# Optimization experiments

Hardware: AMD Instinct MI355X
Metric: run time of the kernel (lower is better)

The kernel has to match this reference:

```python
import jax, jax.numpy as jnp
import numpy as np

IN_CHANNELS = 512
NUM_HEADS = 8
HEAD_CH = IN_CHANNELS // NUM_HEADS


def setup_inputs() -> dict:
    key = jax.random.key(0)
    k0, k1, k2, k3, k4 = jax.random.split(key, 5)
    B, C, H, W = 4, IN_CHANNELS, 128, 128
    x = jax.random.normal(k0, (B, C, H, W), dtype=jnp.float32)
    # 1x1 Conv2d weights == per-pixel linear layers over channels
    s_in = 1.0 / np.sqrt(C)
    Wqkv = jax.random.uniform(k1, (3 * C, C), dtype=jnp.float32, minval=-s_in, maxval=s_in)
    bqkv = jax.random.uniform(k2, (3 * C,), dtype=jnp.float32, minval=-s_in, maxval=s_in)
    Wout = jax.random.uniform(k3, (C, C), dtype=jnp.float32, minval=-s_in, maxval=s_in)
    bout = jax.random.uniform(k4, (C,), dtype=jnp.float32, minval=-s_in, maxval=s_in)
    return {"x": x, "Wqkv": Wqkv, "bqkv": bqkv, "Wout": Wout, "bout": bout}


def _axial_attention(x, Wqkv, bqkv, Wout, bout):
    B, C, H, W = x.shape
    nh, d = NUM_HEADS, HEAD_CH
    scale = 1.0 / jnp.sqrt(jnp.asarray(d, dtype=x.dtype))

    # 1x1 conv qkv projection: [B, 3C, H, W]
    qkv = jnp.einsum('bchw,oc->bohw', x, Wqkv) + bqkv[None, :, None, None]
    q, k, v = jnp.split(qkv, 3, axis=1)
    # [B, nh, d, H, W]
    q = q.reshape(B, nh, d, H, W)
    k = k.reshape(B, nh, d, H, W)
    v = v.reshape(B, nh, d, H, W)

    # Row attention: for each row h, attend across width (w over u)
    scores_row = jnp.einsum('bndhw,bndhu->bnhwu', q, k) * scale  # [B,nh,H,W,W]
    probs_row = jax.nn.softmax(scores_row, axis=-1)
    out_row = jnp.einsum('bnhwu,bndhu->bndhw', probs_row, v)  # [B,nh,d,H,W]

    # Column attention: for each column w, attend across height (h over g)
    scores_col = jnp.einsum('bndhw,bndgw->bnwhg', q, k) * scale  # [B,nh,W,H,H]
    probs_col = jax.nn.softmax(scores_col, axis=-1)
    out_col = jnp.einsum('bnwhg,bndgw->bndhw', probs_col, v)  # [B,nh,d,H,W]

    out = (out_row + out_col).reshape(B, C, H, W)
    # 1x1 conv output projection
    return jnp.einsum('bchw,oc->bohw', out, Wout) + bout[None, :, None, None]


def reference(x, Wqkv, bqkv, Wout, bout):
    return _axial_attention(x, Wqkv, bqkv, Wout, bout)
```

## Files before the change

kernel.cpp:

```cpp
#include <hip/hip_runtime.h>

#define DI __device__ __forceinline__

typedef __attribute__((ext_vector_type(4))) float f32x4;
typedef __attribute__((ext_vector_type(8))) short s16x8;
typedef __attribute__((ext_vector_type(4))) short s16x4;
typedef unsigned short u16;

#define AS_G(p) ((const __attribute__((address_space(1))) void*)(p))
#define AS_L(p) ((__attribute__((address_space(3))) void*)(p))

DI short f2bf(float f) {
  union { float f; unsigned u; } v; v.f = f;
  unsigned r = v.u + 0x7FFFu + ((v.u >> 16) & 1u);
  return (short)(r >> 16);
}
DI float bf2f(short h) {
  union { unsigned u; float f; } v; v.u = ((unsigned)(u16)h) << 16; return v.f;
}

#define MFMA(a, b, c) __builtin_amdgcn_mfma_f32_16x16x32_bf16((a), (b), (c), 0, 0, 0)

__global__ void cast_weights_kernel(const float* __restrict__ wqkv, u16* __restrict__ wqkv_bf,
                                    const float* __restrict__ wout, u16* __restrict__ wout_bf) {
  const int n1 = 1536 * 512 / 4, n2 = 512 * 512 / 4;
  for (int c = blockIdx.x * blockDim.x + threadIdx.x; c < n1 + n2; c += gridDim.x * blockDim.x) {
    const float4* src; u16* dst; int idx;
    if (c < n1) { src = (const float4*)wqkv; dst = wqkv_bf; idx = c; }
    else        { src = (const float4*)wout; dst = wout_bf; idx = c - n1; }
    float4 v = src[idx];
    s16x4 o;
    o[0] = f2bf(v.x); o[1] = f2bf(v.y); o[2] = f2bf(v.z); o[3] = f2bf(v.w);
    *(s16x4*)(dst + (long)idx * 4) = o;
  }
}

template<bool IN_F32>
__global__ __launch_bounds__(256)
void transpose_kernel(const void* __restrict__ in, u16* __restrict__ out,
                      int in_rstride, int out_rstride, long plane_in, long plane_out) {
  __shared__ __align__(16) u16 t[64][72];
  const int tid = threadIdx.x;
  const long bi = (long)blockIdx.z * plane_in;
  const long bo = (long)blockIdx.z * plane_out;
  const int r0 = blockIdx.y * 64, c0 = blockIdx.x * 64;
#pragma unroll
  for (int i = 0; i < 4; ++i) {
    int c = tid + i * 256;
    int row = c >> 4, c4 = c & 15;
    s16x4 pk;
    if (IN_F32) {
      const float4 v = *(const float4*)((const float*)in + bi + (long)(r0 + row) * in_rstride + c0 + c4 * 4);
      pk[0] = f2bf(v.x); pk[1] = f2bf(v.y); pk[2] = f2bf(v.z); pk[3] = f2bf(v.w);
    } else {
      pk = *(const s16x4*)((const u16*)in + bi + (long)(r0 + row) * in_rstride + c0 + c4 * 4);
    }
    *(s16x4*)&t[row][c4 * 4] = pk;
  }
  __syncthreads();
#pragma unroll
  for (int i = 0; i < 2; ++i) {
    int c = tid + i * 256;
    int orow = c >> 3, u = c & 7;
    s16x8 pk;
#pragma unroll
    for (int j = 0; j < 8; ++j) pk[j] = (short)t[u * 8 + j][orow];
    *(s16x8*)(out + bo + (long)(c0 + orow) * out_rstride + r0 + u * 8) = pk;
  }
}

template<int EPI>
__global__ __launch_bounds__(512, 2)
void gemm_kernel(const u16* __restrict__ A, const u16* __restrict__ B,
                 const float* __restrict__ bias,
                 u16* __restrict__ out_qk, u16* __restrict__ out_v,
                 float* __restrict__ out_f) {
  __shared__ __align__(16) u16 smem[65536];
  const int tid = threadIdx.x;
  const int lane = tid & 63, wid = tid >> 6;
  const int l15 = lane & 15, g4 = lane >> 4;
  const int wr = wid >> 2, wc = wid & 3;
  const int m0 = blockIdx.y * 256, n0 = blockIdx.x * 256;
  const int z = blockIdx.z;
  const u16* Bp = B + (long)z * 8388608;

  f32x4 acc[8][4];
#pragma unroll
  for (int i = 0; i < 8; ++i)
#pragma unroll
    for (int j = 0; j < 4; ++j) { f32x4 z4 = {0.f, 0.f, 0.f, 0.f}; acc[i][j] = z4; }

  auto stage = [&](int kt, int buf) {
    u16* As = smem + buf * 32768;
    u16* Bs = As + 16384;
#pragma unroll
    for (int i = 0; i < 4; ++i) {
      int unit = tid + i * 512;
      int row = unit >> 3;
      int csw = ((unit & 7) ^ (row & 7)) * 8;
      __builtin_amdgcn_global_load_lds(AS_G(A + (long)(m0 + row) * 512 + kt * 64 + csw),
                                       AS_L(As + unit * 8), 16, 0, 0);
    }
#pragma unroll
    for (int i = 0; i < 4; ++i) {
      int unit = tid + i * 512;
      int row = unit >> 3;
      int csw = ((unit & 7) ^ (row & 7)) * 8;
      __builtin_amdgcn_global_load_lds(AS_G(Bp + (long)(n0 + row) * 512 + kt * 64 + csw),
                                       AS_L(Bs + unit * 8), 16, 0, 0);
    }
  };

  stage(0, 0);
  __syncthreads();
#pragma unroll 2
  for (int kt = 0; kt < 8; ++kt) {
    const int cur = kt & 1;
    if (kt < 7) {
      stage(kt + 1, cur ^ 1);
      __builtin_amdgcn_sched_barrier(0);
      asm volatile("s_waitcnt vmcnt(8)" ::: "memory");
    } else {
      asm volatile("s_waitcnt vmcnt(0)" ::: "memory");
    }
    __builtin_amdgcn_s_barrier();
    __builtin_amdgcn_sched_barrier(0);
    const u16* As = smem + cur * 32768;
    const u16* Bs = As + 16384;
#pragma unroll
    for (int ks = 0; ks < 2; ++ks) {
      s16x8 af[8], bfr[4];
#pragma unroll
      for (int mi = 0; mi < 8; ++mi) {
        int row = wr * 128 + mi * 16 + l15;
        af[mi] = *(const s16x8*)(As + row * 64 + (((ks * 4 + g4) ^ (row & 7)) * 8));
      }
#pragma unroll
      for (int ni = 0; ni < 4; ++ni) {
        int row = wc * 64 + ni * 16 + l15;
        bfr[ni] = *(const s16x8*)(Bs + row * 64 + (((ks * 4 + g4) ^ (row & 7)) * 8));
      }
#pragma unroll
      for (int mi = 0; mi < 8; ++mi)
#pragma unroll
        for (int ni = 0; ni < 4; ++ni)
          acc[mi][ni] = MFMA(af[mi], bfr[ni], acc[mi][ni]);
    }
    __builtin_amdgcn_s_barrier();
  }
  __syncthreads();

  u16* tile = smem;
  float* tilef = (float*)smem;

  if (EPI == 0) {
    u16* qk_b = out_qk + (long)z * 16777216;
    u16* v_b  = out_v + (long)z * 8388608;
    if (m0 < 1024) {
#pragma unroll
      for (int pass = 0; pass < 2; ++pass) {
        if (pass) __syncthreads();
        if ((wc >> 1) == pass) {
#pragma unroll
          for (int mi = 0; mi < 8; ++mi) {
            int ol = wr * 128 + mi * 16 + 4 * g4;
            int o0 = m0 + ol;
            float b0 = bias[o0], b1 = bias[o0 + 1], b2 = bias[o0 + 2], b3 = bias[o0 + 3];
#pragma unroll
            for (int ni = 0; ni < 4; ++ni) {
              int pl = (wc & 1) * 64 + ni * 16 + l15;
              s16x4 pk;
              pk[0] = f2bf(acc[mi][ni][0] + b0);
              pk[1] = f2bf(acc[mi][ni][1] + b1);
              pk[2] = f2bf(acc[mi][ni][2] + b2);
              pk[3] = f2bf(acc[mi][ni][3] + b3);
              *(s16x4*)(tile + pl * 264 + ol) = pk;
            }
          }
        }
        __syncthreads();
#pragma unroll
        for (int i = 0; i < 8; ++i) {
          int unit = tid + i * 512;
          int row = unit >> 5, c8 = (unit & 31) * 8;
          s16x8 vr = *(const s16x8*)(tile + row * 264 + c8);
          *(s16x8*)(qk_b + (long)(n0 + pass * 128 + row) * 1024 + m0 + c8) = vr;
        }
      }
    } else {
#pragma unroll
      for (int pass = 0; pass < 2; ++pass) {
        if (pass) __syncthreads();
        if (wr == pass) {
#pragma unroll
          for (int mi = 0; mi < 8; ++mi) {
            int cll = mi * 16 + 4 * g4;
            int o0 = m0 + wr * 128 + cll;
#pragma unroll
            for (int ni = 0; ni < 4; ++ni) {
              int pl = wc * 64 + ni * 16 + l15;
#pragma unroll
              for (int r = 0; r < 4; ++r)
                tile[(cll + r) * 264 + pl] = (u16)f2bf(acc[mi][ni][r] + bias[o0 + r]);
            }
          }
        }
        __syncthreads();
#pragma unroll
        for (int i = 0; i < 8; ++i) {
          int unit = tid + i * 512;
          int row = unit >> 5, c8 = (unit & 31) * 8;
          s16x8 vr = *(const s16x8*)(tile + row * 264 + c8);
          *(s16x8*)(v_b + (long)(m0 - 1024 + pass * 128 + row) * 16384 + n0 + c8) = vr;
        }
      }
    }
  } else {
    float* of = out_f + (long)z * 8388608;
#pragma unroll
    for (int pass = 0; pass < 4; ++pass) {
      if (pass) __syncthreads();
      if (wr == (pass >> 1)) {
#pragma unroll
        for (int mi2 = 0; mi2 < 4; ++mi2) {
          int mi = (pass & 1) * 4 + mi2;
          int oll = mi2 * 16 + 4 * g4;
          int o0 = m0 + wr * 128 + mi * 16 + 4 * g4;
          float bb[4] = {bias[o0], bias[o0 + 1], bias[o0 + 2], bias[o0 + 3]};
#pragma unroll
          for (int ni = 0; ni < 4; ++ni) {
            int pl = wc * 64 + ni * 16 + l15;
#pragma unroll
            for (int r = 0; r < 4; ++r)
              tilef[(oll + r) * 264 + pl] = acc[mi][ni][r] + bb[r];
          }
        }
      }
      __syncthreads();
#pragma unroll
      for (int i = 0; i < 8; ++i) {
        int unit = tid + i * 512;
        int row = unit >> 6, c4 = (unit & 63) * 4;
        f32x4 vr = *(const f32x4*)(tilef + row * 264 + c4);
        *(f32x4*)(of + (long)(m0 + pass * 64 + row) * 16384 + n0 + c4) = vr;
      }
    }
  }
}

template<int MODE>
__global__ __launch_bounds__(512, 2)
void attn_kernel(const u16* __restrict__ qk_t_g, const u16* __restrict__ vsrc_g,
                 u16* __restrict__ outp_g) {
  __shared__ __align__(16) u16 smem[24576];
  u16* qT = smem;
  u16* kT = smem + 8192;
  u16* vS = smem + 16384;
  u16* P  = smem;

  const int tid = threadIdx.x;
  const int lane = tid & 63, wid = tid >> 6;
  const int l15 = lane & 15, g4 = lane >> 4;
  const int b = blockIdx.x >> 10;
  const int gidx = blockIdx.x & 1023;
  const int n = gidx >> 7, pos = gidx & 127;

  const u16* qk_t = qk_t_g + (long)b * 16777216;
  const u16* vsrc = vsrc_g + (long)b * 8388608;
  u16* outp = outp_g + (long)b * 8388608;

  long q_base, q_rstride;
  if (MODE == 0) { q_base = (long)pos * 128 * 1024 + n * 64; q_rstride = 1024; }
  else           { q_base = (long)pos * 1024 + n * 64;       q_rstride = 128 * 1024; }
  const long v_base = (long)n * 64 * 16384 + (long)pos * 128;

#pragma unroll
  for (int j = 0; j < 6; ++j) {
    int t = wid + j * 8;
    if (t < 32) {
      int which = t >> 4;
      int tt = t & 15;
      int row = tt * 8 + (lane >> 3);
      int u = lane & 7;
      const u16* src = qk_t + q_base + which * 512 + (long)row * q_rstride + ((u ^ (row & 7)) * 8);
      __builtin_amdgcn_global_load_lds(AS_G(src), AS_L(smem + t * 512), 16, 0, 0);
    } else {
      int tt = t - 32;
      int row = tt * 4 + (lane >> 4);
      int u = lane & 15;
      const u16* src = vsrc + v_base + (long)row * 16384 + ((u ^ (row & 15)) * 8);
      __builtin_amdgcn_global_load_lds(AS_G(src), AS_L(smem + t * 512), 16, 0, 0);
    }
  }
  __syncthreads();

  f32x4 acc[8];
#pragma unroll
  for (int nt = 0; nt < 8; ++nt) { f32x4 zz = {0.f, 0.f, 0.f, 0.f}; acc[nt] = zz; }
  s16x8 aq[2];
  {
    int row = wid * 16 + l15;
#pragma unroll
    for (int ks = 0; ks < 2; ++ks)
      aq[ks] = *(const s16x8*)(qT + row * 64 + (((ks * 4 + g4) ^ (row & 7)) * 8));
  }
#pragma unroll
  for (int nt = 0; nt < 8; ++nt) {
    int rowk = nt * 16 + l15;
#pragma unroll
    for (int ks = 0; ks < 2; ++ks) {
      s16x8 bk = *(const s16x8*)(kT + rowk * 64 + (((ks * 4 + g4) ^ (rowk & 7)) * 8));
      acc[nt] = MFMA(aq[ks], bk, acc[nt]);
    }
  }

#pragma unroll
  for (int r = 0; r < 4; ++r) {
    float m = -1e30f;
#pragma unroll
    for (int nt = 0; nt < 8; ++nt) m = fmaxf(m, acc[nt][r]);
    m = fmaxf(m, __shfl_xor(m, 1));
    m = fmaxf(m, __shfl_xor(m, 2));
    m = fmaxf(m, __shfl_xor(m, 4));
    m = fmaxf(m, __shfl_xor(m, 8));
    float s = 0.f;
#pragma unroll
    for (int nt = 0; nt < 8; ++nt) {
      float e = __expf((acc[nt][r] - m) * 0.125f);
      acc[nt][r] = e; s += e;
    }
    s += __shfl_xor(s, 1); s += __shfl_xor(s, 2);
    s += __shfl_xor(s, 4); s += __shfl_xor(s, 8);
    float rinv = 1.0f / s;
#pragma unroll
    for (int nt = 0; nt < 8; ++nt) acc[nt][r] *= rinv;
  }
  __syncthreads();

#pragma unroll
  for (int nt = 0; nt < 8; ++nt) {
    int u = nt * 16 + l15;
#pragma unroll
    for (int r = 0; r < 4; ++r) {
      int w = wid * 16 + 4 * g4 + r;
      int ch = (u >> 3) ^ (w & 15);
      P[w * 128 + ch * 8 + (u & 7)] = (u16)f2bf(acc[nt][r]);
    }
  }
  __syncthreads();

  const int mw = wid >> 2, nw = wid & 3;
  f32x4 pacc[2][2];
#pragma unroll
  for (int mi = 0; mi < 2; ++mi)
#pragma unroll
    for (int ni = 0; ni < 2; ++ni) { f32x4 zz = {0.f, 0.f, 0.f, 0.f}; pacc[mi][ni] = zz; }
#pragma unroll
  for (int ks = 0; ks < 4; ++ks) {
    s16x8 av[2], bp[2];
#pragma unroll
    for (int mi = 0; mi < 2; ++mi) {
      int d = (mw * 2 + mi) * 16 + l15;
      av[mi] = *(const s16x8*)(vS + d * 128 + (((ks * 4 + g4) ^ (d & 15)) * 8));
    }
#pragma unroll
    for (int ni = 0; ni < 2; ++ni) {
      int w = (nw * 2 + ni) * 16 + l15;
      bp[ni] = *(const s16x8*)(P + w * 128 + (((ks * 4 + g4) ^ (w & 15)) * 8));
    }
#pragma unroll
    for (int mi = 0; mi < 2; ++mi)
#pragma unroll
      for (int ni = 0; ni < 2; ++ni)
        pacc[mi][ni] = MFMA(av[mi], bp[ni], pacc[mi][ni]);
  }

  long out_pbase, out_pstr;
  if (MODE == 0) { out_pbase = (long)pos * 128 * 512; out_pstr = 512; }
  else           { out_pbase = (long)pos * 512;       out_pstr = 128 * 512; }
#pragma unroll
  for (int mi = 0; mi < 2; ++mi) {
    int d0 = (mw * 2 + mi) * 16 + 4 * g4;
#pragma unroll
    for (int ni = 0; ni < 2; ++ni) {
      int nj = (nw * 2 + ni) * 16 + l15;
      long base = out_pbase + (long)nj * out_pstr + n * 64 + d0;
      if (MODE == 0) {
        s16x4 pk;
#pragma unroll
        for (int r = 0; r < 4; ++r) pk[r] = f2bf(pacc[mi][ni][r]);
        *(s16x4*)(outp + base) = pk;
      } else {
        s16x4 old = *(const s16x4*)(outp + base);
        s16x4 pk;
#pragma unroll
        for (int r = 0; r < 4; ++r) pk[r] = f2bf(bf2f(old[r]) + pacc[mi][ni][r]);
        *(s16x4*)(outp + base) = pk;
      }
    }
  }
}

extern "C" void kernel_launch(void* const* d_in, const int* in_sizes, int n_in,
                              void* d_out, int out_size, void* d_ws, size_t ws_size,
                              hipStream_t stream) {
  const float* x    = (const float*)d_in[0];
  const float* wqkv = (const float*)d_in[1];
  const float* bqkv = (const float*)d_in[2];
  const float* wout = (const float*)d_in[3];
  const float* bout = (const float*)d_in[4];
  float* out = (float*)d_out;

  char* ws = (char*)d_ws;
  size_t off = 0;
  auto alloc = [&](size_t bytes) { void* p = ws + off; off += (bytes + 255) & ~(size_t)255; return p; };
  u16* wqkv_bf = (u16*)alloc(1536L * 512 * 2);
  u16* wout_bf = (u16*)alloc(512L * 512 * 2);
  u16* xT      = (u16*)alloc(4L * 16384 * 512 * 2);
  u16* qk_t    = (u16*)alloc(4L * 16384 * 1024 * 2);
  u16* v_buf   = (u16*)alloc(4L * 512 * 16384 * 2);
  u16* vT      = (u16*)alloc(4L * 512 * 16384 * 2);
  u16* attn_T  = (u16*)alloc(4L * 16384 * 512 * 2);

  cast_weights_kernel<<<256, 256, 0, stream>>>(wqkv, wqkv_bf, wout, wout_bf);
  transpose_kernel<true><<<dim3(256, 8, 4), 256, 0, stream>>>(
      x, xT, 16384, 512, 512L * 16384, 16384L * 512);
  gemm_kernel<0><<<dim3(64, 6, 4), 512, 0, stream>>>(wqkv_bf, xT, bqkv, qk_t, v_buf, nullptr);
  transpose_kernel<false><<<dim3(2, 2, 2048), 256, 0, stream>>>(v_buf, vT, 128, 128, 16384, 16384);
  attn_kernel<0><<<dim3(4096), 512, 0, stream>>>(qk_t, v_buf, attn_T);
  attn_kernel<1><<<dim3(4096), 512, 0, stream>>>(qk_t, vT, attn_T);
  gemm_kernel<1><<<dim3(64, 2, 4), 512, 0, stream>>>(wout_bf, attn_T, bout, nullptr, nullptr, out);
}
```

Baseline: 399.5 us.

## Split GEMM k-tile into four MFMA phases with interleaved staging and setprio

Result: slower. 408.7 us (+2.3%).

```diff
diff --git a/kernel.cpp b/kernel.cpp
--- a/kernel.cpp
+++ b/kernel.cpp
@@ -90,9 +90,8 @@
 #pragma unroll
     for (int j = 0; j < 4; ++j) { f32x4 z4 = {0.f, 0.f, 0.f, 0.f}; acc[i][j] = z4; }
 
-  auto stage = [&](int kt, int buf) {
+  auto stageA = [&](int kt, int buf) {
     u16* As = smem + buf * 32768;
-    u16* Bs = As + 16384;
 #pragma unroll
     for (int i = 0; i < 4; ++i) {
       int unit = tid + i * 512;
@@ -101,6 +100,9 @@
       __builtin_amdgcn_global_load_lds(AS_G(A + (long)(m0 + row) * 512 + kt * 64 + csw),
                                        AS_L(As + unit * 8), 16, 0, 0);
     }
+  };
+  auto stageB = [&](int kt, int buf) {
+    u16* Bs = smem + buf * 32768 + 16384;
 #pragma unroll
     for (int i = 0; i < 4; ++i) {
       int unit = tid + i * 512;
@@ -111,42 +113,53 @@
     }
   };
 
-  stage(0, 0);
-  __syncthreads();
+  stageA(0, 0);
+  stageB(0, 0);
 #pragma unroll 2
-  for (int kt = 0; kt < 8; ++kt) {
-    const int cur = kt & 1;
-    if (kt < 7) {
-      stage(kt + 1, cur ^ 1);
-      __builtin_amdgcn_sched_barrier(0);
-      asm volatile("s_waitcnt vmcnt(8)" ::: "memory");
-    } else {
-      asm volatile("s_waitcnt vmcnt(0)" ::: "memory");
-    }
-    __builtin_amdgcn_s_barrier();
-    __builtin_amdgcn_sched_barrier(0);
+  for (int t = 0; t < 8; ++t) {
+    const int cur = t & 1;
     const u16* As = smem + cur * 32768;
     const u16* Bs = As + 16384;
 #pragma unroll
-    for (int ks = 0; ks < 2; ++ks) {
-      s16x8 af[8], bfr[4];
-#pragma unroll
-      for (int mi = 0; mi < 8; ++mi) {
-        int row = wr * 128 + mi * 16 + l15;
-        af[mi] = *(const s16x8*)(As + row * 64 + (((ks * 4 + g4) ^ (row & 7)) * 8));
+    for (int p = 0; p < 4; ++p) {
+      if (p == 0) {
+        asm volatile("s_waitcnt vmcnt(0)" ::: "memory");
+        __builtin_amdgcn_s_barrier();
+        __builtin_amdgcn_sched_barrier(0);
+      }
+      if (t < 7) {
+        if (p == 0) stageA(t + 1, cur ^ 1);
+        else if (p == 1) stageB(t + 1, cur ^ 1);
+      }
+      s16x8 af[2][2], bfr[4][2];
+#pragma unroll
+      for (int mi2 = 0; mi2 < 2; ++mi2) {
+        int row = wr * 128 + (p * 2 + mi2) * 16 + l15;
+#pragma unroll
+        for (int ks = 0; ks < 2; ++ks)
+          af[mi2][ks] = *(const s16x8*)(As + row * 64 + (((ks * 4 + g4) ^ (row & 7)) * 8));
       }
 #pragma unroll
       for (int ni = 0; ni < 4; ++ni) {
         int row = wc * 64 + ni * 16 + l15;
-        bfr[ni] = *(const s16x8*)(Bs + row * 64 + (((ks * 4 + g4) ^ (row & 7)) * 8));
-      }
-#pragma unroll
-      for (int mi = 0; mi < 8; ++mi)
-#pragma unroll
-        for (int ni = 0; ni < 4; ++ni)
-          acc[mi][ni] = MFMA(af[mi], bfr[ni], acc[mi][ni]);
-    }
-    __builtin_amdgcn_s_barrier();
+#pragma unroll
+        for (int ks = 0; ks < 2; ++ks)
+          bfr[ni][ks] = *(const s16x8*)(Bs + row * 64 + (((ks * 4 + g4) ^ (row & 7)) * 8));
+      }
+      __builtin_amdgcn_s_barrier();
+      asm volatile("s_waitcnt lgkmcnt(0)" ::: "memory");
+      __builtin_amdgcn_sched_barrier(0);
+      __builtin_amdgcn_s_setprio(1);
+#pragma unroll
+      for (int ks = 0; ks < 2; ++ks)
+#pragma unroll
+        for (int mi2 = 0; mi2 < 2; ++mi2)
+#pragma unroll
+          for (int ni = 0; ni < 4; ++ni)
+            acc[p * 2 + mi2][ni] = MFMA(af[mi2][ks], bfr[ni][ks], acc[p * 2 + mi2][ni]);
+      __builtin_amdgcn_s_setprio(0);
+      __builtin_amdgcn_s_barrier();
+    }
   }
   __syncthreads();
 
```
